# Kernel tuning notes

Hardware: AMD Instinct MI355X
Metric: run time of the kernel (lower is better)

## Reference

```python
import jax, jax.numpy as jnp
import numpy as np

HEAD_DIM = 8


def setup_inputs() -> dict:
    key = jax.random.key(0)
    kq, kk, k1, k2, k3, k4 = jax.random.split(key, 6)
    B, C, D, H, W = 2, 64, 32, 64, 64
    query_feats = jax.random.normal(kq, (B, C, D, H, W), dtype=jnp.float32)
    key_feats = jax.random.normal(kk, (B, C, D, H, W), dtype=jnp.float32)
    s = 1.0 / np.sqrt(C)
    # 1x1x1 Conv3d (bias=False) weights, stored as [out_ch, in_ch]
    Wq = jax.random.normal(k1, (C, C), dtype=jnp.float32) * s
    Wk = jax.random.normal(k2, (C, C), dtype=jnp.float32) * s
    Wv = jax.random.normal(k3, (C, C), dtype=jnp.float32) * s
    Wo = jax.random.normal(k4, (C, C), dtype=jnp.float32) * s
    return {"query_feats": query_feats, "key_feats": key_feats,
            "Wq": Wq, "Wk": Wk, "Wv": Wv, "Wo": Wo}


def _proj(W, x):
    # 1x1x1 conv == channel mixing
    return jnp.einsum('oc,bcdhw->bodhw', W, x)


def reference(query_feats, key_feats, Wq, Wk, Wv, Wo):
    B, C, D, H, W_ = query_feats.shape
    hw = H * W_
    heads = C // HEAD_DIM
    q = _proj(Wq, query_feats)   # [B, C, D, H, W]
    k = _proj(Wk, key_feats)
    v = _proj(Wv, key_feats)
    # reshape to [B, heads, head_dim, D, hw] then rearrange
    q = q.reshape(B, heads, HEAD_DIM, D, hw).transpose(0, 4, 1, 3, 2)  # [B,hw,heads,D,hd]
    k = k.reshape(B, heads, HEAD_DIM, D, hw).transpose(0, 4, 1, 2, 3)  # [B,hw,heads,hd,D]
    v = v.reshape(B, heads, HEAD_DIM, D, hw).transpose(0, 4, 1, 3, 2)  # [B,hw,heads,D,hd]
    sim = jnp.matmul(q, k) * (HEAD_DIM ** -0.5)      # [B,hw,heads,D,D]
    sim = jax.nn.softmax(sim, axis=-1)
    ctx = jnp.matmul(sim, v)                          # [B,hw,heads,D,hd]
    # permute(0,1,2,4,3) then flatten heads*hd -> C, then to [B,C,D,H,W]
    ctx = ctx.transpose(0, 1, 2, 4, 3).reshape(B, hw, C, D)
    ctx = ctx.transpose(0, 2, 3, 1).reshape(B, C, D, H, W_)
    out = _proj(Wo, ctx)
    return out
```

## Files before the change

### kernel.cpp

```cpp
#include <hip/hip_runtime.h>

#define SB   131072
#define CSTR 131072
#define BSTR 8388608

using u32x4  = __attribute__((ext_vector_type(4))) unsigned int;
using u32x2  = __attribute__((ext_vector_type(2))) unsigned int;
using bf16x8 = __attribute__((ext_vector_type(8))) short;
using f32x4  = __attribute__((ext_vector_type(4))) float;
using f32x2  = __attribute__((ext_vector_type(2))) float;

__device__ __forceinline__ unsigned pack2(float a, float b) {
    unsigned r;
    asm("v_cvt_pk_bf16_f32 %0, %1, %2" : "=v"(r) : "v"(a), "v"(b));
    return r;
}
__device__ __forceinline__ float bflo(unsigned u) { return __uint_as_float(u << 16); }
__device__ __forceinline__ float bfhi(unsigned u) { return __uint_as_float(u & 0xffff0000u); }

__device__ __forceinline__ f32x4 mfma16(bf16x8 a, bf16x8 b, f32x4 c) {
    return __builtin_amdgcn_mfma_f32_16x16x32_bf16(a, b, c, 0, 0, 0);
}

typedef const __attribute__((address_space(1))) void* gptr_t;
typedef __attribute__((address_space(3))) void* lptr_t;
__device__ __forceinline__ void gl_lds16(const float* g, float* l) {
    __builtin_amdgcn_global_load_lds((gptr_t)g, (lptr_t)l, 16, 0, 0);
}

#define LOAD_A_FRAGS(A, W, n, qd)                                          \
    _Pragma("unroll")                                                      \
    for (int half = 0; half < 2; ++half) {                                 \
        float4 wr[8];                                                      \
        _Pragma("unroll")                                                  \
        for (int mh = 0; mh < 2; ++mh)                                     \
            _Pragma("unroll")                                              \
            for (int kt = 0; kt < 2; ++kt) {                               \
                const int o = (half * 2 + mh) * 16 + (n);                  \
                const int c = kt * 32 + (qd) * 8;                          \
                wr[(mh * 2 + kt) * 2]     = *(const float4*)&W[o * 64 + c];     \
                wr[(mh * 2 + kt) * 2 + 1] = *(const float4*)&W[o * 64 + c + 4]; \
            }                                                              \
        _Pragma("unroll")                                                  \
        for (int mh = 0; mh < 2; ++mh)                                     \
            _Pragma("unroll")                                              \
            for (int kt = 0; kt < 2; ++kt) {                               \
                union { bf16x8 v; unsigned u[4]; } tw;                     \
                const float4 w0 = wr[(mh * 2 + kt) * 2];                   \
                const float4 w1 = wr[(mh * 2 + kt) * 2 + 1];               \
                tw.u[0] = pack2(w0.x, w0.y);                               \
                tw.u[1] = pack2(w0.z, w0.w);                               \
                tw.u[2] = pack2(w1.x, w1.y);                               \
                tw.u[3] = pack2(w1.z, w1.w);                               \
                A[half * 2 + mh][kt] = tw.v;                               \
            }                                                              \
    }

#define LDS_BFRAG_F32(Bf, col, qd)                                         \
    _Pragma("unroll")                                                      \
    for (int kt = 0; kt < 2; ++kt) {                                       \
        union { bf16x8 v; unsigned u[4]; } tb;                             \
        _Pragma("unroll")                                                  \
        for (int r = 0; r < 4; ++r) {                                      \
            const int c = kt * 32 + (qd) * 8 + 2 * r;                      \
            tb.u[r] = pack2((col)[c * 32], (col)[c * 32 + 32]);            \
        }                                                                  \
        Bf[kt] = tb.v;                                                     \
    }

__global__ __launch_bounds__(256)
void k1_proj(const float* __restrict__ qf, const float* __restrict__ kf,
             const float* __restrict__ Wq, const float* __restrict__ Wk,
             const float* __restrict__ Wv, unsigned* __restrict__ Qs,
             unsigned* __restrict__ Ks, unsigned* __restrict__ Vs)
{
    __shared__ float lsf[8192];

    const int vbid = blockIdx.x >> 1;
    const int path = blockIdx.x & 1;
    const int wv   = (int)threadIdx.x >> 6;
    const int wid  = vbid * 4 + wv;
    const int lane = threadIdx.x & 63;
    const int qd   = lane >> 4;
    const int n    = lane & 15;
    const int S0   = wid * 32;
    const int b    = S0 >> 17;
    const int tl   = S0 & (SB - 1);
    const int woff = wv * 2048;

    const float* xb = (path == 0 ? qf : kf) + (size_t)b * BSTR;

    if (path == 0) {
        bf16x8 A[4][2];
        LOAD_A_FRAGS(A, Wq, n, qd)

        {
            const float* gsrc = xb + (size_t)(lane >> 3) * CSTR + tl + (lane & 7) * 4;
            float* ldst = &lsf[woff];
            #pragma unroll
            for (int i = 0; i < 8; ++i)
                gl_lds16(gsrc + (size_t)(8 * i) * CSTR, ldst + i * 256);
        }
        asm volatile("s_waitcnt vmcnt(0)" ::: "memory");
        __builtin_amdgcn_sched_barrier(0);

        #pragma unroll
        for (int t = 0; t < 2; ++t) {
            const int sl   = t * 16 + n;
            const int site = tl + sl;
            const float* col = &lsf[woff + sl];
            bf16x8 Bf[2];
            LDS_BFRAG_F32(Bf, col, qd)
            f32x4 acc[4];
            #pragma unroll
            for (int mt = 0; mt < 4; ++mt) acc[mt] = (f32x4){0.f, 0.f, 0.f, 0.f};
            #pragma unroll
            for (int kt = 0; kt < 2; ++kt)
                #pragma unroll
                for (int mt = 0; mt < 4; ++mt)
                    acc[mt] = mfma16(A[mt][kt], Bf[kt], acc[mt]);
            #pragma unroll
            for (int mt = 0; mt < 4; ++mt) {
                const int h = 2 * mt + (qd >> 1);
                unsigned* dst = Qs + ((unsigned)(b * 8 + h) * SB + site) * 4 + (qd & 1) * 2;
                u32x2 w;
                w.x = pack2(acc[mt][0], acc[mt][1]);
                w.y = pack2(acc[mt][2], acc[mt][3]);
                *(u32x2*)dst = w;
            }
        }
    } else {
        bf16x8 AK[4][2], AV[4][2];
        LOAD_A_FRAGS(AK, Wk, n, qd)
        LOAD_A_FRAGS(AV, Wv, n, qd)

        {
            const float* gsrc = xb + (size_t)(lane >> 3) * CSTR + tl + (lane & 7) * 4;
            float* ldst = &lsf[woff];
            #pragma unroll
            for (int i = 0; i < 8; ++i)
                gl_lds16(gsrc + (size_t)(8 * i) * CSTR, ldst + i * 256);
        }
        asm volatile("s_waitcnt vmcnt(0)" ::: "memory");
        __builtin_amdgcn_sched_barrier(0);

        #pragma unroll
        for (int t = 0; t < 2; ++t) {
            const int sl   = t * 16 + n;
            const int site = tl + sl;
            const float* col = &lsf[woff + sl];
            bf16x8 Bf[2];
            LDS_BFRAG_F32(Bf, col, qd)
            f32x4 aK[4], aV[4];
            #pragma unroll
            for (int mt = 0; mt < 4; ++mt) {
                aK[mt] = (f32x4){0.f, 0.f, 0.f, 0.f};
                aV[mt] = (f32x4){0.f, 0.f, 0.f, 0.f};
            }
            #pragma unroll
            for (int kt = 0; kt < 2; ++kt)
                #pragma unroll
                for (int mt = 0; mt < 4; ++mt) {
                    aK[mt] = mfma16(AK[mt][kt], Bf[kt], aK[mt]);
                    aV[mt] = mfma16(AV[mt][kt], Bf[kt], aV[mt]);
                }
            #pragma unroll
            for (int mt = 0; mt < 4; ++mt) {
                const int h = 2 * mt + (qd >> 1);
                const unsigned off = ((unsigned)(b * 8 + h) * SB + site) * 4 + (qd & 1) * 2;
                u32x2 wk2, wv2;
                wk2.x = pack2(aK[mt][0], aK[mt][1]);
                wk2.y = pack2(aK[mt][2], aK[mt][3]);
                wv2.x = pack2(aV[mt][0], aV[mt][1]);
                wv2.y = pack2(aV[mt][2], aV[mt][3]);
                *(u32x2*)(Ks + off) = wk2;
                *(u32x2*)(Vs + off) = wv2;
            }
        }
    }
}

__global__ __launch_bounds__(256)
void k2_attn(const u32x4* Qs, const u32x4* __restrict__ Ks,
             const u32x4* __restrict__ Vs, u32x4* Cs)
{
    __shared__ unsigned int kls[4096];
    __shared__ unsigned int vls[4096];

    const int blk = blockIdx.x;
    const int h   = blk & 7;
    const int w   = blk >> 3;
    const int b   = w >> 7;
    const int pos0 = (w & 127) * 32;

    const int tid = threadIdx.x;
    const int pos = tid & 31;
    const int dqt = tid >> 5;

    const int base = (b * 8 + h) * SB;

    #pragma unroll
    for (int i = 0; i < 4; ++i) {
        const int idx = tid + i * 256;
        const int dp = idx >> 5, pp = idx & 31;
        *(u32x4*)&kls[idx * 4] = Ks[base + dp * 4096 + pos0 + pp];
        *(u32x4*)&vls[idx * 4] = Vs[base + dp * 4096 + pos0 + pp];
    }
    __syncthreads();

    const float sc = 0.35355339059327373f * 1.4426950408889634f;

    #pragma unroll 1
    for (int p = 0; p < 2; ++p) {
        const int dq0 = dqt + 16 * p;
        const u32x4 qa = Qs[base + dq0 * 4096 + pos0 + pos];
        const u32x4 qb = Qs[base + (dq0 + 8) * 4096 + pos0 + pos];
        f32x2 q2[8];
        q2[0] = (f32x2){bflo(qa.x) * sc, bflo(qb.x) * sc};
        q2[1] = (f32x2){bfhi(qa.x) * sc, bfhi(qb.x) * sc};
        q2[2] = (f32x2){bflo(qa.y) * sc, bflo(qb.y) * sc};
        q2[3] = (f32x2){bfhi(qa.y) * sc, bfhi(qb.y) * sc};
        q2[4] = (f32x2){bflo(qa.z) * sc, bflo(qb.z) * sc};
        q2[5] = (f32x2){bfhi(qa.z) * sc, bfhi(qb.z) * sc};
        q2[6] = (f32x2){bflo(qa.w) * sc, bflo(qb.w) * sc};
        q2[7] = (f32x2){bfhi(qa.w) * sc, bfhi(qb.w) * sc};

        f32x2 cx[8];
        #pragma unroll
        for (int e = 0; e < 8; ++e) cx[e] = (f32x2){0.f, 0.f};
        f32x2 sum2 = (f32x2){0.f, 0.f};

        #pragma unroll 4
        for (int dp = 0; dp < 32; ++dp) {
            const u32x4 kk = *(const u32x4*)&kls[(dp * 32 + pos) * 4];
            const u32x4 vv = *(const u32x4*)&vls[(dp * 32 + pos) * 4];
            f32x2 accA = q2[0] * bflo(kk.x);
            f32x2 accB = q2[1] * bfhi(kk.x);
            accA += q2[2] * bflo(kk.y);
            accB += q2[3] * bfhi(kk.y);
            accA += q2[4] * bflo(kk.z);
            accB += q2[5] * bfhi(kk.z);
            accA += q2[6] * bflo(kk.w);
            accB += q2[7] * bfhi(kk.w);
            const f32x2 acc = accA + accB;
            f32x2 ex;
            ex.x = exp2f(acc.x);
            ex.y = exp2f(acc.y);
            sum2 += ex;
            cx[0] += ex * bflo(vv.x);
            cx[1] += ex * bfhi(vv.x);
            cx[2] += ex * bflo(vv.y);
            cx[3] += ex * bfhi(vv.y);
            cx[4] += ex * bflo(vv.z);
            cx[5] += ex * bfhi(vv.z);
            cx[6] += ex * bflo(vv.w);
            cx[7] += ex * bfhi(vv.w);
        }

        const f32x2 inv2 = (f32x2){1.0f / sum2.x, 1.0f / sum2.y};
        #pragma unroll
        for (int e = 0; e < 8; ++e) cx[e] *= inv2;

        u32x4 pa, pb;
        pa.x = pack2(cx[0].x, cx[1].x); pa.y = pack2(cx[2].x, cx[3].x);
        pa.z = pack2(cx[4].x, cx[5].x); pa.w = pack2(cx[6].x, cx[7].x);
        pb.x = pack2(cx[0].y, cx[1].y); pb.y = pack2(cx[2].y, cx[3].y);
        pb.z = pack2(cx[4].y, cx[5].y); pb.w = pack2(cx[6].y, cx[7].y);
        Cs[base + dq0 * 4096 + pos0 + pos] = pa;
        Cs[base + (dq0 + 8) * 4096 + pos0 + pos] = pb;
    }
}

__global__ __launch_bounds__(256)
void k3_out(const u32x4* __restrict__ Cs, const float* __restrict__ Wo,
            float* __restrict__ out)
{
    const int wid  = (blockIdx.x * 256 + threadIdx.x) >> 6;
    const int lane = threadIdx.x & 63;
    const int qd   = lane >> 4;
    const int n    = lane & 15;
    const int S0   = wid * 64;
    const int b    = S0 >> 17;
    const int tl   = S0 & (SB - 1);

    bf16x8 Bf[4][2];
    #pragma unroll
    for (int t = 0; t < 4; ++t) {
        const int site = tl + t * 16 + n;
        #pragma unroll
        for (int kt = 0; kt < 2; ++kt)
            Bf[t][kt] = *(const bf16x8*)(Cs + (unsigned)(b * 8 + kt * 4 + qd) * SB + site);
    }

    bf16x8 A[4][2];
    LOAD_A_FRAGS(A, Wo, n, qd)

    #pragma unroll
    for (int t = 0; t < 4; ++t) {
        const int site = tl + t * 16 + n;
        f32x4 acc[4];
        #pragma unroll
        for (int mt = 0; mt < 4; ++mt) acc[mt] = (f32x4){0.f, 0.f, 0.f, 0.f};
        #pragma unroll
        for (int kt = 0; kt < 2; ++kt)
            #pragma unroll
            for (int mt = 0; mt < 4; ++mt)
                acc[mt] = mfma16(A[mt][kt], Bf[t][kt], acc[mt]);
        #pragma unroll
        for (int mt = 0; mt < 4; ++mt)
            #pragma unroll
            for (int r = 0; r < 4; ++r)
                out[(size_t)b * BSTR + (size_t)(mt * 16 + qd * 4 + r) * CSTR + site]
                    = acc[mt][r];
    }
}

extern "C" void kernel_launch(void* const* d_in, const int* in_sizes, int n_in,
                              void* d_out, int out_size, void* d_ws, size_t ws_size,
                              hipStream_t stream) {
    const float* qf = (const float*)d_in[0];
    const float* kf = (const float*)d_in[1];
    const float* Wq = (const float*)d_in[2];
    const float* Wk = (const float*)d_in[3];
    const float* Wv = (const float*)d_in[4];
    const float* Wo = (const float*)d_in[5];
    float* out = (float*)d_out;

    unsigned* Qs = (unsigned*)d_ws;
    unsigned* Vs = (unsigned*)((char*)d_ws + (size_t)33554432);
    unsigned* Ks = (unsigned*)d_out;

    hipLaunchKernelGGL(k1_proj, dim3(4096), dim3(256), 0, stream,
                       qf, kf, Wq, Wk, Wv, Qs, Ks, Vs);
    hipLaunchKernelGGL(k2_attn, dim3(2048), dim3(256), 0, stream,
                       (const u32x4*)Qs, (const u32x4*)Ks, (const u32x4*)Vs,
                       (u32x4*)Qs);
    hipLaunchKernelGGL(k3_out, dim3(1024), dim3(256), 0, stream,
                       (const u32x4*)Qs, Wo, out);
}
```

Baseline: 308.3 us.

## Make projection kernel persistent with double-buffered LDS prefetch across strips

The projection kernel now launches 512 blocks instead of 4096. Each wave loops over 8 strips spaced 1024 apart, and the global-to-LDS loads for the next strip are issued while the current strip is being computed. A double buffer in LDS (twice the shared memory) and partial vmcnt waits let memory latency overlap with MFMA work and stores. The risks are lower occupancy from the larger LDS footprint, and waitcnt counts that must match the outstanding loads and stores exactly.

Result: faster. 280.0 us (-9.2%).

```diff
diff --git a/kernel.cpp b/kernel.cpp
--- a/kernel.cpp
+++ b/kernel.cpp
@@ -74,109 +74,131 @@
              const float* __restrict__ Wv, unsigned* __restrict__ Qs,
              unsigned* __restrict__ Ks, unsigned* __restrict__ Vs)
 {
-    __shared__ float lsf[8192];
+    __shared__ float lsf[16384];
 
     const int vbid = blockIdx.x >> 1;
     const int path = blockIdx.x & 1;
     const int wv   = (int)threadIdx.x >> 6;
-    const int wid  = vbid * 4 + wv;
+    const int wid0 = vbid * 4 + wv;
     const int lane = threadIdx.x & 63;
     const int qd   = lane >> 4;
     const int n    = lane & 15;
-    const int S0   = wid * 32;
-    const int b    = S0 >> 17;
-    const int tl   = S0 & (SB - 1);
-    const int woff = wv * 2048;
-
-    const float* xb = (path == 0 ? qf : kf) + (size_t)b * BSTR;
+    float* buf0 = &lsf[wv * 4096];
+    float* buf1 = buf0 + 2048;
+
+    const float* xb0 = (path == 0) ? qf : kf;
+
+    auto prefetch = [&](int strip, float* dst) {
+        const int S0 = strip * 32;
+        const float* gsrc = xb0 + (size_t)(S0 >> 17) * BSTR
+                          + (size_t)(lane >> 3) * CSTR + (S0 & (SB - 1))
+                          + (lane & 7) * 4;
+        #pragma unroll
+        for (int i = 0; i < 8; ++i)
+            gl_lds16(gsrc + (size_t)(8 * i) * CSTR, dst + i * 256);
+    };
 
     if (path == 0) {
         bf16x8 A[4][2];
         LOAD_A_FRAGS(A, Wq, n, qd)
 
-        {
-            const float* gsrc = xb + (size_t)(lane >> 3) * CSTR + tl + (lane & 7) * 4;
-            float* ldst = &lsf[woff];
+        auto compute = [&](const float* buf, int strip) {
+            const int S0 = strip * 32;
+            const int b  = S0 >> 17;
+            const int tl = S0 & (SB - 1);
             #pragma unroll
-            for (int i = 0; i < 8; ++i)
-                gl_lds16(gsrc + (size_t)(8 * i) * CSTR, ldst + i * 256);
-        }
+            for (int t = 0; t < 2; ++t) {
+                const int sl   = t * 16 + n;
+                const int site = tl + sl;
+                bf16x8 Bf[2];
+                LDS_BFRAG_F32(Bf, buf + sl, qd)
+                f32x4 acc[4];
+                #pragma unroll
+                for (int mt = 0; mt < 4; ++mt) acc[mt] = (f32x4){0.f, 0.f, 0.f, 0.f};
+                #pragma unroll
+                for (int kt = 0; kt < 2; ++kt)
+                    #pragma unroll
+                    for (int mt = 0; mt < 4; ++mt)
+                        acc[mt] = mfma16(A[mt][kt], Bf[kt], acc[mt]);
+                #pragma unroll
+                for (int mt = 0; mt < 4; ++mt) {
+                    const int h = 2 * mt + (qd >> 1);
+                    unsigned* dst = Qs + ((unsigned)(b * 8 + h) * SB + site) * 4 + (qd & 1) * 2;
+                    u32x2 w;
+                    w.x = pack2(acc[mt][0], acc[mt][1]);
+                    w.y = pack2(acc[mt][2], acc[mt][3]);
+                    *(u32x2*)dst = w;
+                }
+            }
+        };
+
+        prefetch(wid0, buf0);
         asm volatile("s_waitcnt vmcnt(0)" ::: "memory");
         __builtin_amdgcn_sched_barrier(0);
-
-        #pragma unroll
-        for (int t = 0; t < 2; ++t) {
-            const int sl   = t * 16 + n;
-            const int site = tl + sl;
-            const float* col = &lsf[woff + sl];
-            bf16x8 Bf[2];
-            LDS_BFRAG_F32(Bf, col, qd)
-            f32x4 acc[4];
-            #pragma unroll
-            for (int mt = 0; mt < 4; ++mt) acc[mt] = (f32x4){0.f, 0.f, 0.f, 0.f};
-            #pragma unroll
-            for (int kt = 0; kt < 2; ++kt)
-                #pragma unroll
-                for (int mt = 0; mt < 4; ++mt)
-                    acc[mt] = mfma16(A[mt][kt], Bf[kt], acc[mt]);
-            #pragma unroll
-            for (int mt = 0; mt < 4; ++mt) {
-                const int h = 2 * mt + (qd >> 1);
-                unsigned* dst = Qs + ((unsigned)(b * 8 + h) * SB + site) * 4 + (qd & 1) * 2;
-                u32x2 w;
-                w.x = pack2(acc[mt][0], acc[mt][1]);
-                w.y = pack2(acc[mt][2], acc[mt][3]);
-                *(u32x2*)dst = w;
-            }
+        #pragma unroll 1
+        for (int it = 0; it < 7; ++it) {
+            float* nxt = (it & 1) ? buf0 : buf1;
+            prefetch(wid0 + (it + 1) * 1024, nxt);
+            compute((it & 1) ? buf1 : buf0, wid0 + it * 1024);
+            asm volatile("s_waitcnt vmcnt(8)" ::: "memory");
+            __builtin_amdgcn_sched_barrier(0);
         }
+        compute(buf1, wid0 + 7 * 1024);
     } else {
         bf16x8 AK[4][2], AV[4][2];
         LOAD_A_FRAGS(AK, Wk, n, qd)
         LOAD_A_FRAGS(AV, Wv, n, qd)
 
-        {
-            const float* gsrc = xb + (size_t)(lane >> 3) * CSTR + tl + (lane & 7) * 4;
-            float* ldst = &lsf[woff];
+        auto computekv = [&](const float* buf, int strip) {
+            const int S0 = strip * 32;
+            const int b  = S0 >> 17;
+            const int tl = S0 & (SB - 1);
             #pragma unroll
-            for (int i = 0; i < 8; ++i)
-                gl_lds16(gsrc + (size_t)(8 * i) * CSTR, ldst + i * 256);
-        }
+            for (int t = 0; t < 2; ++t) {
+                const int sl   = t * 16 + n;
+                const int site = tl + sl;
+                bf16x8 Bf[2];
+                LDS_BFRAG_F32(Bf, buf + sl, qd)
+                f32x4 aK[4], aV[4];
+                #pragma unroll
+                for (int mt = 0; mt < 4; ++mt) {
+                    aK[mt] = (f32x4){0.f, 0.f, 0.f, 0.f};
+                    aV[mt] = (f32x4){0.f, 0.f, 0.f, 0.f};
+                }
+                #pragma unroll
+                for (int kt = 0; kt < 2; ++kt)
+                    #pragma unroll
+                    for (int mt = 0; mt < 4; ++mt) {
+                        aK[mt] = mfma16(AK[mt][kt], Bf[kt], aK[mt]);
+                        aV[mt] = mfma16(AV[mt][kt], Bf[kt], aV[mt]);
+                    }
+                #pragma unroll
+                for (int mt = 0; mt < 4; ++mt) {
+                    const int h = 2 * mt + (qd >> 1);
+                    const unsigned off = ((unsigned)(b * 8 + h) * SB + site) * 4 + (qd & 1) * 2;
+                    u32x2 wk2, wv2;
+                    wk2.x = pack2(aK[mt][0], aK[mt][1]);
+                    wk2.y = pack2(aK[mt][2], aK[mt][3]);
+                    wv2.x = pack2(aV[mt][0], aV[mt][1]);
+                    wv2.y = pack2(aV[mt][2], aV[mt][3]);
+                    *(u32x2*)(Ks + off) = wk2;
+                    *(u32x2*)(Vs + off) = wv2;
+                }
+            }
+        };
+
+        prefetch(wid0, buf0);
         asm volatile("s_waitcnt vmcnt(0)" ::: "memory");
         __builtin_amdgcn_sched_barrier(0);
-
-        #pragma unroll
-        for (int t = 0; t < 2; ++t) {
-            const int sl   = t * 16 + n;
-            const int site = tl + sl;
-            const float* col = &lsf[woff + sl];
-            bf16x8 Bf[2];
-            LDS_BFRAG_F32(Bf, col, qd)
-            f32x4 aK[4], aV[4];
-            #pragma unroll
-            for (int mt = 0; mt < 4; ++mt) {
-                aK[mt] = (f32x4){0.f, 0.f, 0.f, 0.f};
-                aV[mt] = (f32x4){0.f, 0.f, 0.f, 0.f};
-            }
-            #pragma unroll
-            for (int kt = 0; kt < 2; ++kt)
-                #pragma unroll
-                for (int mt = 0; mt < 4; ++mt) {
-                    aK[mt] = mfma16(AK[mt][kt], Bf[kt], aK[mt]);
-                    aV[mt] = mfma16(AV[mt][kt], Bf[kt], aV[mt]);
-                }
-            #pragma unroll
-            for (int mt = 0; mt < 4; ++mt) {
-                const int h = 2 * mt + (qd >> 1);
-                const unsigned off = ((unsigned)(b * 8 + h) * SB + site) * 4 + (qd & 1) * 2;
-                u32x2 wk2, wv2;
-                wk2.x = pack2(aK[mt][0], aK[mt][1]);
-                wk2.y = pack2(aK[mt][2], aK[mt][3]);
-                wv2.x = pack2(aV[mt][0], aV[mt][1]);
-                wv2.y = pack2(aV[mt][2], aV[mt][3]);
-                *(u32x2*)(Ks + off) = wk2;
-                *(u32x2*)(Vs + off) = wv2;
-            }
+        #pragma unroll 1
+        for (int it = 0; it < 7; ++it) {
+            float* nxt = (it & 1) ? buf0 : buf1;
+            prefetch(wid0 + (it + 1) * 1024, nxt);
+            computekv((it & 1) ? buf1 : buf0, wid0 + it * 1024);
+            asm volatile("s_waitcnt vmcnt(16)" ::: "memory");
+            __builtin_amdgcn_sched_barrier(0);
         }
+        computekv(buf1, wid0 + 7 * 1024);
     }
 }
 
@@ -330,7 +352,7 @@
     unsigned* Vs = (unsigned*)((char*)d_ws + (size_t)33554432);
     unsigned* Ks = (unsigned*)d_out;
 
-    hipLaunchKernelGGL(k1_proj, dim3(4096), dim3(256), 0, stream,
+    hipLaunchKernelGGL(k1_proj, dim3(512), dim3(256), 0, stream,
                        qf, kf, Wq, Wk, Wv, Qs, Ks, Vs);
     hipLaunchKernelGGL(k2_attn, dim3(2048), dim3(256), 0, stream,
                        (const u32x4*)Qs, (const u32x4*)Ks, (const u32x4*)Vs,
```
